# Kernel optimization log

Measured on AMD Instinct MI355X. Metric: run time of the kernel, lower is better.

The kernel has to match this reference:

```python
import jax, jax.numpy as jnp
import numpy as np

NUM_HEADS = 16
D_MODEL = 1024
D_K = D_MODEL // NUM_HEADS


def setup_inputs() -> dict:
    key = jax.random.key(0)
    ks = jax.random.split(key, 11)
    B, S, D = 1, 4096, D_MODEL
    scale = 1.0 / np.sqrt(D)
    return {
        "Q": jax.random.normal(ks[0], (B, S, D), jnp.float32),
        "K": jax.random.normal(ks[1], (B, S, D), jnp.float32),
        "V": jax.random.normal(ks[2], (B, S, D), jnp.float32),
        "W_Q": jax.random.normal(ks[3], (D, D), jnp.float32) * scale,
        "b_Q": jax.random.normal(ks[4], (D,), jnp.float32) * 0.02,
        "W_K": jax.random.normal(ks[5], (D, D), jnp.float32) * scale,
        "b_K": jax.random.normal(ks[6], (D,), jnp.float32) * 0.02,
        "W_V": jax.random.normal(ks[7], (D, D), jnp.float32) * scale,
        "b_V": jax.random.normal(ks[8], (D,), jnp.float32) * 0.02,
        "W_O": jax.random.normal(ks[9], (D, D), jnp.float32) * scale,
        "b_O": jax.random.normal(ks[10], (D,), jnp.float32) * 0.02,
    }


def _split_heads(x):
    # (B, S, D) -> (B, H, S, d_k)
    B, S, _ = x.shape
    return x.reshape(B, S, NUM_HEADS, D_K).transpose(0, 2, 1, 3)


def reference(Q, K, V, W_Q, b_Q, W_K, b_K, W_V, b_V, W_O, b_O):
    q = _split_heads(Q @ W_Q + b_Q)  # (B, H, S, d_k)
    k = _split_heads(K @ W_K + b_K)
    v = _split_heads(V @ W_V + b_V)
    inv_sqrt_dk = jnp.asarray(1.0 / np.sqrt(D_K), q.dtype)
    scores = jnp.einsum("bhqd,bhkd->bhqk", q, k) * inv_sqrt_dk  # (B, H, S, S)
    weights = jax.nn.softmax(scores, axis=-1)
    out = jnp.einsum("bhqk,bhkd->bhqd", weights, v)  # (B, H, S, d_k)
    B, _, S, _ = out.shape
    combined = out.transpose(0, 2, 1, 3).reshape(B, S, D_MODEL)
    return combined @ W_O + b_O
```

## Files before the change

### kernel.cpp

```cpp
#include <hip/hip_runtime.h>

typedef float f32x2 __attribute__((ext_vector_type(2)));
typedef float f32x4 __attribute__((ext_vector_type(4)));
typedef float f32x16 __attribute__((ext_vector_type(16)));
typedef short bf16x8 __attribute__((ext_vector_type(8)));
typedef unsigned u32x2 __attribute__((ext_vector_type(2)));
typedef unsigned short u16;

#define S_LEN 4096
#define DMODEL 1024
#define NH 16
#define DK 64

#define SCALE_Q 0.18033688f

static __device__ __forceinline__ u16 f2bf(float x) {
  union { float f; unsigned u; } v; v.f = x;
  unsigned r = v.u + 0x7fffu + ((v.u >> 16) & 1u);
  return (u16)(r >> 16);
}

static __device__ __forceinline__ float bf2f(u16 x) {
  union { unsigned u; float f; } v; v.u = ((unsigned)x) << 16;
  return v.f;
}

#if __has_builtin(__builtin_amdgcn_exp2f)
#define EXP2F __builtin_amdgcn_exp2f
#else
#define EXP2F exp2f
#endif

static __device__ __forceinline__ unsigned pkbf(float lo, float hi) {
  unsigned r;
  asm("v_cvt_pk_bf16_f32 %0, %1, %2" : "=v"(r) : "v"(lo), "v"(hi));
  return r;
}

static __device__ __forceinline__ void plswap(unsigned& a, unsigned& b, int hi) {
#if __has_builtin(__builtin_amdgcn_permlane32_swap)
  u32x2 r = __builtin_amdgcn_permlane32_swap(a, b, false, false);
  a = r.x; b = r.y;
  (void)hi;
#else
  unsigned ax = __shfl_xor(a, 32), bx = __shfl_xor(b, 32);
  unsigned na = hi ? bx : a;
  unsigned nb = hi ? b : ax;
  a = na; b = nb;
#endif
}

static __device__ __forceinline__ void gload16(const void* g, void* l) {
  void* gg = (void*)g;
  __builtin_amdgcn_global_load_lds(
      (__attribute__((address_space(1))) void*)gg,
      (__attribute__((address_space(3))) void*)l, 16, 0, 0);
}

__global__ __launch_bounds__(256) void prep(const float* __restrict__ W0,
                                            const float* __restrict__ W1,
                                            const float* __restrict__ W2,
                                            const float* __restrict__ W3,
                                            u16* __restrict__ Wt,
                                            const float* __restrict__ Q,
                                            const float* __restrict__ K,
                                            const float* __restrict__ V,
                                            u16* __restrict__ Qbf) {
  __shared__ float t[32][33];
  const int b = blockIdx.x;
  const int tid = threadIdx.x;
  if (b < 4096) {
    const int z = b >> 10;
    const int rem = b & 1023;
    const float* W = (z == 0) ? W0 : (z == 1) ? W1 : (z == 2) ? W2 : W3;
    u16* dst = Wt + (size_t)z * DMODEL * DMODEL;
    const int x = tid & 31, y = tid >> 5;
    const int n0 = (rem & 31) * 32, k0 = (rem >> 5) * 32;
#pragma unroll
    for (int i = 0; i < 4; ++i)
      t[y + 8 * i][x] = W[(size_t)(k0 + y + 8 * i) * DMODEL + n0 + x];
    __syncthreads();
#pragma unroll
    for (int i = 0; i < 4; ++i)
      dst[(size_t)(n0 + y + 8 * i) * DMODEL + k0 + x] = f2bf(t[x][y + 8 * i]);
  } else {
    const int b2 = b - 4096;
    const int z = b2 >> 10;
    const int blk = b2 & 1023;
    const float* src = (z == 0) ? Q : (z == 1) ? K : V;
    u16* dst = Qbf + (size_t)z * S_LEN * DMODEL;
    const int n8 = S_LEN * DMODEL / 8;
    for (int i = blk * 256 + tid; i < n8; i += 1024 * 256) {
      float4 a = ((const float4*)src)[2 * i];
      float4 c = ((const float4*)src)[2 * i + 1];
      union { ushort4 u[2]; int4 q; } tt;
      tt.u[0].x = f2bf(a.x); tt.u[0].y = f2bf(a.y);
      tt.u[0].z = f2bf(a.z); tt.u[0].w = f2bf(a.w);
      tt.u[1].x = f2bf(c.x); tt.u[1].y = f2bf(c.y);
      tt.u[1].z = f2bf(c.z); tt.u[1].w = f2bf(c.w);
      ((int4*)dst)[i] = tt.q;
    }
  }
}

template <int MODE>
__global__ __launch_bounds__(256) void pgemm(const u16* __restrict__ Abase,
                                             const u16* __restrict__ Btbase,
                                             const float* __restrict__ bq,
                                             const float* __restrict__ bk,
                                             const float* __restrict__ bv,
                                             void* __restrict__ outbase) {
  __shared__ __align__(16) char Al[16384];
  __shared__ __align__(16) char Bl[16384];
  const int nblk = gridDim.x, cpx = nblk >> 3;
  const int b0 = blockIdx.x;
  const int bid = (b0 & 7) * cpx + (b0 >> 3);
  const int z = (MODE == 0) ? (bid >> 8) : 0;
  const int rem = bid & 255;
  const int nb = rem & 7, mb = rem >> 3;
  const int m0 = mb * 128, n0 = nb * 128;
  const int tid = threadIdx.x, lane = tid & 63, wid = tid >> 6;
  const int l31 = lane & 31, hi = lane >> 5;
  const int wm = (wid >> 1) * 64, wn = (wid & 1) * 64;
  const char* Ab = (const char*)(Abase + (size_t)z * S_LEN * DMODEL);
  const char* Bb = (const char*)(Btbase + (size_t)z * DMODEL * DMODEL);
  const float* bias = (z == 0) ? bq : (z == 1 ? bk : bv);
  const float scale = (MODE == 0 && z == 0) ? SCALE_Q : 1.0f;

  f32x16 acc[2][2] = {};

  for (int kt = 0; kt < 16; ++kt) {
    const int kb = kt * 128;
#pragma unroll
    for (int p = 0; p < 4; ++p) {
      int lin = p * 4096 + tid * 16;
      int row = lin >> 7;
      int colg = (lin & 127) ^ ((row & 7) << 4);
      gload16(Ab + (size_t)(m0 + row) * 2048 + kb + colg,
              Al + p * 4096 + wid * 1024);
    }
#pragma unroll
    for (int p = 0; p < 4; ++p) {
      int lin = p * 4096 + tid * 16;
      int row = lin >> 7;
      int colg = (lin & 127) ^ ((row & 7) << 4);
      gload16(Bb + (size_t)(n0 + row) * 2048 + kb + colg,
              Bl + p * 4096 + wid * 1024);
    }
    __syncthreads();
#pragma unroll
    for (int ks = 0; ks < 4; ++ks) {
      bf16x8 a2[2], b2[2];
#pragma unroll
      for (int f = 0; f < 2; ++f) {
        int row = wm + f * 32 + l31;
        a2[f] = *(const bf16x8*)(Al + row * 128 +
                                 ((ks * 32 + hi * 16) ^ ((row & 7) << 4)));
      }
#pragma unroll
      for (int g = 0; g < 2; ++g) {
        int row = wn + g * 32 + l31;
        b2[g] = *(const bf16x8*)(Bl + row * 128 +
                                 ((ks * 32 + hi * 16) ^ ((row & 7) << 4)));
      }
#pragma unroll
      for (int f = 0; f < 2; ++f)
#pragma unroll
        for (int g = 0; g < 2; ++g)
          acc[f][g] =
              __builtin_amdgcn_mfma_f32_32x32x16_bf16(a2[f], b2[g], acc[f][g], 0, 0, 0);
    }
    __syncthreads();
  }

#pragma unroll
  for (int f = 0; f < 2; ++f) {
#pragma unroll
    for (int g = 0; g < 2; ++g) {
      const int col = n0 + wn + g * 32 + l31;
      const int row0 = m0 + wm + f * 32 + 4 * hi;
      const float bb = bias[col];
      if (MODE == 1) {
        float* of = (float*)outbase;
#pragma unroll
        for (int i = 0; i < 16; ++i) {
          const int row = row0 + (i & 3) + 8 * (i >> 2);
          of[(size_t)row * DMODEL + col] = acc[f][g][i] + bb;
        }
      } else if (z == 2) {
        u16* ov = (u16*)outbase + (size_t)2 * S_LEN * DMODEL;
        u16* base = ov + ((size_t)(col >> 6) * DK + (col & 63)) * S_LEN;
#pragma unroll
        for (int q2 = 0; q2 < 4; ++q2) {
          const int row = row0 + 8 * q2;
          ushort4 u;
          u.x = f2bf(acc[f][g][4 * q2 + 0] + bb);
          u.y = f2bf(acc[f][g][4 * q2 + 1] + bb);
          u.z = f2bf(acc[f][g][4 * q2 + 2] + bb);
          u.w = f2bf(acc[f][g][4 * q2 + 3] + bb);
          *(ushort4*)(base + row) = u;
        }
      } else {
        u16* oq = (u16*)outbase + (size_t)z * S_LEN * DMODEL;
#pragma unroll
        for (int i = 0; i < 16; ++i) {
          const int row = row0 + (i & 3) + 8 * (i >> 2);
          oq[((size_t)(col >> 6) * S_LEN + row) * DK + (col & 63)] =
              f2bf((acc[f][g][i] + bb) * scale);
        }
      }
    }
  }
}

__global__ __launch_bounds__(512) void attn2(const u16* __restrict__ q,
                                             const u16* __restrict__ k,
                                             const u16* __restrict__ vt,
                                             u16* __restrict__ Opart,
                                             float* __restrict__ Lpart) {
  __shared__ __align__(16) char smem[32768];
  const int bid0 = blockIdx.x;
  const int bid = (bid0 & 7) * 64 + (bid0 >> 3);
  const int h = bid >> 5;
  const int kvh = (bid >> 4) & 1;
  const int qblk = bid & 15;
  const int tid = threadIdx.x;
  const int wid = tid >> 6, lane = tid & 63;
  const int l31 = lane & 31, hi = lane >> 5;

  const char* kpb = (const char*)k + (size_t)h * S_LEN * (DK * 2);
  const char* vtb = (const char*)vt + (size_t)h * DK * (S_LEN * 2);

  const int q0w = qblk * 256 + wid * 32;
  const u16* qrow = q + ((size_t)h * S_LEN + q0w + l31) * DK;
  bf16x8 qf[4];
#pragma unroll
  for (int dt = 0; dt < 4; ++dt)
    qf[dt] = *(const bf16x8*)(qrow + dt * 16 + hi * 8);

  f32x16 o0 = {}, o1 = {};
  f32x2 lacc2 = {0.f, 0.f};

  const int woff = wid << 10;
  const int kt0 = kvh * 32;
  const int kt1 = kt0 + 32;

  const int swz = (l31 & 7) << 4;
  int dsa[4];
#pragma unroll
  for (int dt = 0; dt < 4; ++dt)
    dsa[dt] = (l31 << 7) + ((dt * 32 + hi * 16) ^ swz);

  const int lin = tid * 16;
  const int sw = lin ^ (((lin >> 7) & 7) << 4);
  const char* gk = kpb + (size_t)kt0 * 8192 + sw;
  const char* gv = vtb + (size_t)(lin >> 7) * 8192 + (size_t)kt0 * 128 + (sw & 127);

  gload16(gk, smem + woff);          gk += 8192;
  gload16(gv, smem + 8192 + woff);   gv += 128;

  auto body = [&](const int CUR, const int NXT, bool doStage) {
    if (doStage) {
      gload16(gk, smem + NXT + woff);          gk += 8192;
      gload16(gv, smem + NXT + 8192 + woff);   gv += 128;
      asm volatile("s_waitcnt vmcnt(2)" ::: "memory");
    } else {
      asm volatile("s_waitcnt vmcnt(0)" ::: "memory");
    }
    __builtin_amdgcn_s_barrier();

    const char* kb = smem + CUR;
    const char* vb = smem + CUR + 8192;

    f32x16 st0 = {}, st1 = {};
    __builtin_amdgcn_s_setprio(1);
#pragma unroll
    for (int dt = 0; dt < 4; ++dt) {
      bf16x8 k0 = *(const bf16x8*)(kb + dsa[dt]);
      bf16x8 k1 = *(const bf16x8*)(kb + 4096 + dsa[dt]);
      st0 = __builtin_amdgcn_mfma_f32_32x32x16_bf16(k0, qf[dt], st0, 0, 0, 0);
      st1 = __builtin_amdgcn_mfma_f32_32x32x16_bf16(k1, qf[dt], st1, 0, 0, 0);
    }
    __builtin_amdgcn_s_setprio(0);

    unsigned w0[8], w1[8];
    f32x2 s2 = {0.f, 0.f};
#pragma unroll
    for (int i = 0; i < 8; ++i) {
      float a0 = EXP2F(st0[2 * i]), a1 = EXP2F(st0[2 * i + 1]);
      f32x2 t = {a0, a1}; s2 += t;
      w0[i] = pkbf(a0, a1);
    }
#pragma unroll
    for (int i = 0; i < 8; ++i) {
      float a0 = EXP2F(st1[2 * i]), a1 = EXP2F(st1[2 * i + 1]);
      f32x2 t = {a0, a1}; s2 += t;
      w1[i] = pkbf(a0, a1);
    }
    lacc2 += s2;

    union UF { unsigned w[4]; bf16x8 v; };
    UF f[4];
#pragma unroll
    for (int g = 0; g < 2; ++g) {
#pragma unroll
      for (int j = 0; j < 2; ++j) {
        unsigned a = w0[4 * g + j], b = w0[4 * g + j + 2];
        plswap(a, b, hi);
        f[g].w[j] = a; f[g].w[j + 2] = b;
        unsigned c = w1[4 * g + j], d = w1[4 * g + j + 2];
        plswap(c, d, hi);
        f[2 + g].w[j] = c; f[2 + g].w[j + 2] = d;
      }
    }

    __builtin_amdgcn_s_setprio(1);
#pragma unroll
    for (int kt2 = 0; kt2 < 4; ++kt2) {
      bf16x8 v0 = *(const bf16x8*)(vb + dsa[kt2]);
      bf16x8 v1 = *(const bf16x8*)(vb + 4096 + dsa[kt2]);
      o0 = __builtin_amdgcn_mfma_f32_32x32x16_bf16(v0, f[kt2].v, o0, 0, 0, 0);
      o1 = __builtin_amdgcn_mfma_f32_32x32x16_bf16(v1, f[kt2].v, o1, 0, 0, 0);
    }
    __builtin_amdgcn_s_setprio(0);

    __builtin_amdgcn_s_barrier();
  };

  for (int kt = kt0; kt < kt1; kt += 2) {
    body(0, 16384, kt + 1 < kt1);
    body(16384, 0, kt + 2 < kt1);
  }

  const float lacc = lacc2.x + lacc2.y;
  const float lrow = lacc + __shfl_xor(lacc, 32);
  u16* Ob = Opart + ((((size_t)kvh * NH + h) * S_LEN) + q0w + l31) * DK;
#pragma unroll
  for (int g = 0; g < 4; ++g) {
    ushort4 u0, u1;
    u0.x = f2bf(o0[g * 4 + 0]); u0.y = f2bf(o0[g * 4 + 1]);
    u0.z = f2bf(o0[g * 4 + 2]); u0.w = f2bf(o0[g * 4 + 3]);
    *(ushort4*)(Ob + 8 * g + 4 * hi) = u0;
    u1.x = f2bf(o1[g * 4 + 0]); u1.y = f2bf(o1[g * 4 + 1]);
    u1.z = f2bf(o1[g * 4 + 2]); u1.w = f2bf(o1[g * 4 + 3]);
    *(ushort4*)(Ob + 32 + 8 * g + 4 * hi) = u1;
  }
  Lpart[((size_t)kvh * NH + h) * S_LEN + q0w + l31] = lrow;
}

__global__ __launch_bounds__(256) void combine(const u16* __restrict__ Op,
                                               const float* __restrict__ Lp,
                                               u16* __restrict__ comb) {
  const int id = blockIdx.x * 256 + threadIdx.x;
  const int h = id >> 16;
  const int rem = id & 65535;
  const int qv = rem >> 4;
  const int d4 = (rem & 15) << 2;
  const size_t str = (size_t)NH * S_LEN * DK;
  const size_t base = (((size_t)h * S_LEN) + qv) * DK + d4;
  float o0 = 0.f, o1 = 0.f, o2 = 0.f, o3 = 0.f, l = 0.f;
#pragma unroll
  for (int kv = 0; kv < 2; ++kv) {
    ushort4 u = *(const ushort4*)(Op + kv * str + base);
    o0 += bf2f(u.x); o1 += bf2f(u.y); o2 += bf2f(u.z); o3 += bf2f(u.w);
    l += Lp[(size_t)kv * NH * S_LEN + (size_t)h * S_LEN + qv];
  }
  const float inv = 1.f / l;
  ushort4 u;
  u.x = f2bf(o0 * inv);
  u.y = f2bf(o1 * inv);
  u.z = f2bf(o2 * inv);
  u.w = f2bf(o3 * inv);
  *(ushort4*)(comb + (size_t)qv * DMODEL + h * DK + d4) = u;
}

extern "C" void kernel_launch(void* const* d_in, const int* in_sizes, int n_in,
                              void* d_out, int out_size, void* d_ws, size_t ws_size,
                              hipStream_t stream) {
  (void)in_sizes; (void)n_in; (void)out_size; (void)ws_size;
  const float* Q   = (const float*)d_in[0];
  const float* K   = (const float*)d_in[1];
  const float* V   = (const float*)d_in[2];
  const float* W_Q = (const float*)d_in[3];
  const float* b_Q = (const float*)d_in[4];
  const float* W_K = (const float*)d_in[5];
  const float* b_K = (const float*)d_in[6];
  const float* W_V = (const float*)d_in[7];
  const float* b_V = (const float*)d_in[8];
  const float* W_O = (const float*)d_in[9];
  const float* b_O = (const float*)d_in[10];
  float* out = (float*)d_out;

  char* ws = (char*)d_ws;
  const size_t MB = 1024 * 1024;
  u16* WtQ = (u16*)ws;
  u16* Qbf = (u16*)(ws + 8 * MB);
  u16* Opart = (u16*)(ws + 8 * MB);
  u16* qp   = (u16*)(ws + 40 * MB);
  u16* kp   = qp + (size_t)S_LEN * DMODEL;
  u16* vtp  = kp + (size_t)S_LEN * DMODEL;
  u16* comb = vtp + (size_t)S_LEN * DMODEL;
  float* Lpart = (float*)(ws + 72 * MB);

  prep<<<7168, 256, 0, stream>>>(W_Q, W_K, W_V, W_O, WtQ, Q, K, V, Qbf);

  pgemm<0><<<768, 256, 0, stream>>>(Qbf, WtQ, b_Q, b_K, b_V, qp);

  attn2<<<512, 512, 0, stream>>>(qp, kp, vtp, Opart, Lpart);
  combine<<<4096, 256, 0, stream>>>(Opart, Lpart, comb);

  pgemm<1><<<256, 256, 0, stream>>>(comb, WtQ + (size_t)3 * DMODEL * DMODEL,
                                    b_O, b_O, b_O, out);
}
```

Baseline: 164.4 us.

## Double attention KV stage depth and add dedicated output-projection GEMM

The attention kernel now stages two 64-key tiles per barrier pair, using 64KB of LDS, so each pair of barriers covers twice the compute and synchronisation overhead per key is halved. Separately, the final output projection moves from the generic pgemm<1> to a new ogemm kernel with 64x128 tiles and 512 blocks, meant to fill more CUs. The larger LDS footprint may lower attention occupancy, and ogemm is not pipelined, synchronising twice per k-step.

```diff
diff --git a/kernel.cpp b/kernel.cpp
--- a/kernel.cpp
+++ b/kernel.cpp
@@ -213,12 +213,81 @@
   }
 }
 
+__global__ __launch_bounds__(256) void ogemm(const u16* __restrict__ A,
+                                             const u16* __restrict__ Bt,
+                                             const float* __restrict__ bias,
+                                             float* __restrict__ out) {
+  __shared__ __align__(16) char Al[8192];
+  __shared__ __align__(16) char Bl[16384];
+  const int b0 = blockIdx.x;
+  const int bid = (b0 & 7) * 64 + (b0 >> 3);
+  const int nb = bid & 7, mb = bid >> 3;
+  const int m0 = mb * 64, n0 = nb * 128;
+  const int tid = threadIdx.x, lane = tid & 63, wid = tid >> 6;
+  const int l31 = lane & 31, hi = lane >> 5;
+  const int wm = (wid >> 1) * 32, wn = (wid & 1) * 64;
+  const char* Ab = (const char*)A;
+  const char* Bb = (const char*)Bt;
+
+  f32x16 acc[2] = {};
+
+  for (int kt = 0; kt < 16; ++kt) {
+    const int kb = kt * 128;
+#pragma unroll
+    for (int p = 0; p < 2; ++p) {
+      int lin = p * 4096 + tid * 16;
+      int row = lin >> 7;
+      int colg = (lin & 127) ^ ((row & 7) << 4);
+      gload16(Ab + (size_t)(m0 + row) * 2048 + kb + colg,
+              Al + p * 4096 + wid * 1024);
+    }
+#pragma unroll
+    for (int p = 0; p < 4; ++p) {
+      int lin = p * 4096 + tid * 16;
+      int row = lin >> 7;
+      int colg = (lin & 127) ^ ((row & 7) << 4);
+      gload16(Bb + (size_t)(n0 + row) * 2048 + kb + colg,
+              Bl + p * 4096 + wid * 1024);
+    }
+    __syncthreads();
+#pragma unroll
+    for (int ks = 0; ks < 4; ++ks) {
+      int rowA = wm + l31;
+      bf16x8 a2 = *(const bf16x8*)(Al + rowA * 128 +
+                                   ((ks * 32 + hi * 16) ^ ((rowA & 7) << 4)));
+      bf16x8 b2[2];
+#pragma unroll
+      for (int g = 0; g < 2; ++g) {
+        int row = wn + g * 32 + l31;
+        b2[g] = *(const bf16x8*)(Bl + row * 128 +
+                                 ((ks * 32 + hi * 16) ^ ((row & 7) << 4)));
+      }
+#pragma unroll
+      for (int g = 0; g < 2; ++g)
+        acc[g] = __builtin_amdgcn_mfma_f32_32x32x16_bf16(a2, b2[g], acc[g], 0, 0, 0);
+    }
+    __syncthreads();
+  }
+
+#pragma unroll
+  for (int g = 0; g < 2; ++g) {
+    const int col = n0 + wn + g * 32 + l31;
+    const int row0 = m0 + wm + 4 * hi;
+    const float bb = bias[col];
+#pragma unroll
+    for (int i = 0; i < 16; ++i) {
+      const int row = row0 + (i & 3) + 8 * (i >> 2);
+      out[(size_t)row * DMODEL + col] = acc[g][i] + bb;
+    }
+  }
+}
+
 __global__ __launch_bounds__(512) void attn2(const u16* __restrict__ q,
                                              const u16* __restrict__ k,
                                              const u16* __restrict__ vt,
                                              u16* __restrict__ Opart,
                                              float* __restrict__ Lpart) {
-  __shared__ __align__(16) char smem[32768];
+  __shared__ __align__(16) char smem[65536];
   const int bid0 = blockIdx.x;
   const int bid = (bid0 & 7) * 64 + (bid0 >> 3);
   const int h = bid >> 5;
@@ -243,7 +312,6 @@
 
   const int woff = wid << 10;
   const int kt0 = kvh * 32;
-  const int kt1 = kt0 + 32;
 
   const int swz = (l31 & 7) << 4;
   int dsa[4];
@@ -256,22 +324,14 @@
   const char* gk = kpb + (size_t)kt0 * 8192 + sw;
   const char* gv = vtb + (size_t)(lin >> 7) * 8192 + (size_t)kt0 * 128 + (sw & 127);
 
-  gload16(gk, smem + woff);          gk += 8192;
-  gload16(gv, smem + 8192 + woff);   gv += 128;
-
-  auto body = [&](const int CUR, const int NXT, bool doStage) {
-    if (doStage) {
-      gload16(gk, smem + NXT + woff);          gk += 8192;
-      gload16(gv, smem + NXT + 8192 + woff);   gv += 128;
-      asm volatile("s_waitcnt vmcnt(2)" ::: "memory");
-    } else {
-      asm volatile("s_waitcnt vmcnt(0)" ::: "memory");
-    }
-    __builtin_amdgcn_s_barrier();
-
-    const char* kb = smem + CUR;
-    const char* vb = smem + CUR + 8192;
-
+  gload16(gk, smem + woff);           gk += 8192;
+  gload16(gv, smem + 8192 + woff);    gv += 128;
+  gload16(gk, smem + 16384 + woff);   gk += 8192;
+  gload16(gv, smem + 24576 + woff);   gv += 128;
+
+  union UF { unsigned w[4]; bf16x8 v; };
+
+  auto subtile = [&](const char* kb, const char* vb) {
     f32x16 st0 = {}, st1 = {};
     __builtin_amdgcn_s_setprio(1);
 #pragma unroll
@@ -299,7 +359,6 @@
     }
     lacc2 += s2;
 
-    union UF { unsigned w[4]; bf16x8 v; };
     UF f[4];
 #pragma unroll
     for (int g = 0; g < 2; ++g) {
@@ -323,13 +382,29 @@
       o1 = __builtin_amdgcn_mfma_f32_32x32x16_bf16(v1, f[kt2].v, o1, 0, 0, 0);
     }
     __builtin_amdgcn_s_setprio(0);
+  };
+
+  auto body = [&](const int CUR, const int NXT, bool doStage) {
+    if (doStage) {
+      gload16(gk, smem + NXT + woff);           gk += 8192;
+      gload16(gv, smem + NXT + 8192 + woff);    gv += 128;
+      gload16(gk, smem + NXT + 16384 + woff);   gk += 8192;
+      gload16(gv, smem + NXT + 24576 + woff);   gv += 128;
+      asm volatile("s_waitcnt vmcnt(4)" ::: "memory");
+    } else {
+      asm volatile("s_waitcnt vmcnt(0)" ::: "memory");
+    }
+    __builtin_amdgcn_s_barrier();
+
+    subtile(smem + CUR, smem + CUR + 8192);
+    subtile(smem + CUR + 16384, smem + CUR + 24576);
 
     __builtin_amdgcn_s_barrier();
   };
 
-  for (int kt = kt0; kt < kt1; kt += 2) {
-    body(0, 16384, kt + 1 < kt1);
-    body(16384, 0, kt + 2 < kt1);
+  for (int b2 = 0; b2 < 16; b2 += 2) {
+    body(0, 32768, b2 + 1 < 16);
+    body(32768, 0, b2 + 2 < 16);
   }
 
   const float lacc = lacc2.x + lacc2.y;
@@ -409,6 +484,6 @@
   attn2<<<512, 512, 0, stream>>>(qp, kp, vtp, Opart, Lpart);
   combine<<<4096, 256, 0, stream>>>(Opart, Lpart, comb);
 
-  pgemm<1><<<256, 256, 0, stream>>>(comb, WtQ + (size_t)3 * DMODEL * DMODEL,
-                                    b_O, b_O, b_O, out);
-}
+  ogemm<<<512, 256, 0, stream>>>(comb, WtQ + (size_t)3 * DMODEL * DMODEL,
+                                 b_O, out);
+}
```

New measurement: 161.8 us. No clear change (-1.6%).

## Double-buffer LDS in projection GEMM and add smaller-tile output GEMM

Applied to the files above, without the earlier changes.

The QKV projection GEMM now double-buffers its A/B tiles in LDS. It issues the next k-tile's global-to-LDS loads before computing the current one, with explicit vmcnt waits and barriers replacing the load-sync-compute-sync loop. The output projection moves to a dedicated kernel with 64x128 tiles and 512 blocks for better CU occupancy on the 256-tile problem, also double-buffered. LDS per block grows to 64KB and 48KB, which may limit blocks per CU, and the hand-placed waitcnt counts must match the exact load counts.

```diff
diff --git a/kernel.cpp b/kernel.cpp
--- a/kernel.cpp
+++ b/kernel.cpp
@@ -103,19 +103,17 @@
   }
 }
 
-template <int MODE>
 __global__ __launch_bounds__(256) void pgemm(const u16* __restrict__ Abase,
                                              const u16* __restrict__ Btbase,
                                              const float* __restrict__ bq,
                                              const float* __restrict__ bk,
                                              const float* __restrict__ bv,
                                              void* __restrict__ outbase) {
-  __shared__ __align__(16) char Al[16384];
-  __shared__ __align__(16) char Bl[16384];
+  __shared__ __align__(16) char smem[65536];
   const int nblk = gridDim.x, cpx = nblk >> 3;
   const int b0 = blockIdx.x;
   const int bid = (b0 & 7) * cpx + (b0 >> 3);
-  const int z = (MODE == 0) ? (bid >> 8) : 0;
+  const int z = bid >> 8;
   const int rem = bid & 255;
   const int nb = rem & 7, mb = rem >> 3;
   const int m0 = mb * 128, n0 = nb * 128;
@@ -125,29 +123,34 @@
   const char* Ab = (const char*)(Abase + (size_t)z * S_LEN * DMODEL);
   const char* Bb = (const char*)(Btbase + (size_t)z * DMODEL * DMODEL);
   const float* bias = (z == 0) ? bq : (z == 1 ? bk : bv);
-  const float scale = (MODE == 0 && z == 0) ? SCALE_Q : 1.0f;
+  const float scale = (z == 0) ? SCALE_Q : 1.0f;
 
   f32x16 acc[2][2] = {};
 
-  for (int kt = 0; kt < 16; ++kt) {
-    const int kb = kt * 128;
-#pragma unroll
-    for (int p = 0; p < 4; ++p) {
-      int lin = p * 4096 + tid * 16;
-      int row = lin >> 7;
-      int colg = (lin & 127) ^ ((row & 7) << 4);
-      gload16(Ab + (size_t)(m0 + row) * 2048 + kb + colg,
-              Al + p * 4096 + wid * 1024);
-    }
-#pragma unroll
-    for (int p = 0; p < 4; ++p) {
-      int lin = p * 4096 + tid * 16;
-      int row = lin >> 7;
-      int colg = (lin & 127) ^ ((row & 7) << 4);
-      gload16(Bb + (size_t)(n0 + row) * 2048 + kb + colg,
-              Bl + p * 4096 + wid * 1024);
-    }
-    __syncthreads();
+  float bb2[2];
+#pragma unroll
+  for (int g = 0; g < 2; ++g) bb2[g] = bias[n0 + wn + g * 32 + l31];
+  asm volatile("s_waitcnt vmcnt(0)" ::: "memory");
+
+  const int r8 = tid >> 3;
+  const int colg = ((tid * 16) & 127) ^ ((r8 & 7) << 4);
+  const char* gA = Ab + (size_t)(m0 + r8) * 2048 + colg;
+  const char* gB = Bb + (size_t)(n0 + r8) * 2048 + colg;
+  const int ldst = wid * 1024;
+
+  auto stageAB = [&](int base) {
+#pragma unroll
+    for (int p = 0; p < 4; ++p)
+      gload16(gA + p * 65536, smem + base + p * 4096 + ldst);
+#pragma unroll
+    for (int p = 0; p < 4; ++p)
+      gload16(gB + p * 65536, smem + base + 16384 + p * 4096 + ldst);
+    gA += 128; gB += 128;
+  };
+
+  auto compute = [&](int base) {
+    const char* Al = smem + base;
+    const char* Bl = smem + base + 16384;
 #pragma unroll
     for (int ks = 0; ks < 4; ++ks) {
       bf16x8 a2[2], b2[2];
@@ -170,7 +173,25 @@
           acc[f][g] =
               __builtin_amdgcn_mfma_f32_32x32x16_bf16(a2[f], b2[g], acc[f][g], 0, 0, 0);
     }
-    __syncthreads();
+  };
+
+  auto body = [&](const int CUR, const int NXT, bool doStage) {
+    __builtin_amdgcn_sched_barrier(0);
+    if (doStage) {
+      stageAB(NXT);
+      asm volatile("s_waitcnt vmcnt(8)" ::: "memory");
+    } else {
+      asm volatile("s_waitcnt vmcnt(0)" ::: "memory");
+    }
+    __builtin_amdgcn_s_barrier();
+    compute(CUR);
+    __builtin_amdgcn_s_barrier();
+  };
+
+  stageAB(0);
+  for (int kt = 0; kt < 16; kt += 2) {
+    body(0, 32768, kt + 1 < 16);
+    body(32768, 0, kt + 2 < 16);
   }
 
 #pragma unroll
@@ -179,15 +200,8 @@
     for (int g = 0; g < 2; ++g) {
       const int col = n0 + wn + g * 32 + l31;
       const int row0 = m0 + wm + f * 32 + 4 * hi;
-      const float bb = bias[col];
-      if (MODE == 1) {
-        float* of = (float*)outbase;
-#pragma unroll
-        for (int i = 0; i < 16; ++i) {
-          const int row = row0 + (i & 3) + 8 * (i >> 2);
-          of[(size_t)row * DMODEL + col] = acc[f][g][i] + bb;
-        }
-      } else if (z == 2) {
+      const float bb = bb2[g];
+      if (z == 2) {
         u16* ov = (u16*)outbase + (size_t)2 * S_LEN * DMODEL;
         u16* base = ov + ((size_t)(col >> 6) * DK + (col & 63)) * S_LEN;
 #pragma unroll
@@ -209,6 +223,95 @@
               f2bf((acc[f][g][i] + bb) * scale);
         }
       }
+    }
+  }
+}
+
+__global__ __launch_bounds__(256) void ogemm(const u16* __restrict__ A,
+                                             const u16* __restrict__ Bt,
+                                             const float* __restrict__ bias,
+                                             float* __restrict__ out) {
+  __shared__ __align__(16) char smem[49152];
+  const int b0 = blockIdx.x;
+  const int bid = (b0 & 7) * 64 + (b0 >> 3);
+  const int nb = bid & 7, mb = bid >> 3;
+  const int m0 = mb * 64, n0 = nb * 128;
+  const int tid = threadIdx.x, lane = tid & 63, wid = tid >> 6;
+  const int l31 = lane & 31, hi = lane >> 5;
+  const int wm = (wid >> 1) * 32, wn = (wid & 1) * 64;
+
+  f32x16 acc[2] = {};
+
+  float bb2[2];
+#pragma unroll
+  for (int g = 0; g < 2; ++g) bb2[g] = bias[n0 + wn + g * 32 + l31];
+  asm volatile("s_waitcnt vmcnt(0)" ::: "memory");
+
+  const int r8 = tid >> 3;
+  const int colg = ((tid * 16) & 127) ^ ((r8 & 7) << 4);
+  const char* gA = (const char*)A + (size_t)(m0 + r8) * 2048 + colg;
+  const char* gB = (const char*)Bt + (size_t)(n0 + r8) * 2048 + colg;
+  const int ldst = wid * 1024;
+
+  auto stageAB = [&](int base) {
+#pragma unroll
+    for (int p = 0; p < 2; ++p)
+      gload16(gA + p * 65536, smem + base + p * 4096 + ldst);
+#pragma unroll
+    for (int p = 0; p < 4; ++p)
+      gload16(gB + p * 65536, smem + base + 8192 + p * 4096 + ldst);
+    gA += 128; gB += 128;
+  };
+
+  auto compute = [&](int base) {
+    const char* Al = smem + base;
+    const char* Bl = smem + base + 8192;
+#pragma unroll
+    for (int ks = 0; ks < 4; ++ks) {
+      int rowA = wm + l31;
+      bf16x8 a2 = *(const bf16x8*)(Al + rowA * 128 +
+                                   ((ks * 32 + hi * 16) ^ ((rowA & 7) << 4)));
+      bf16x8 b2[2];
+#pragma unroll
+      for (int g = 0; g < 2; ++g) {
+        int row = wn + g * 32 + l31;
+        b2[g] = *(const bf16x8*)(Bl + row * 128 +
+                                 ((ks * 32 + hi * 16) ^ ((row & 7) << 4)));
+      }
+#pragma unroll
+      for (int g = 0; g < 2; ++g)
+        acc[g] = __builtin_amdgcn_mfma_f32_32x32x16_bf16(a2, b2[g], acc[g], 0, 0, 0);
+    }
+  };
+
+  auto body = [&](const int CUR, const int NXT, bool doStage) {
+    __builtin_amdgcn_sched_barrier(0);
+    if (doStage) {
+      stageAB(NXT);
+      asm volatile("s_waitcnt vmcnt(6)" ::: "memory");
+    } else {
+      asm volatile("s_waitcnt vmcnt(0)" ::: "memory");
+    }
+    __builtin_amdgcn_s_barrier();
+    compute(CUR);
+    __builtin_amdgcn_s_barrier();
+  };
+
+  stageAB(0);
+  for (int kt = 0; kt < 16; kt += 2) {
+    body(0, 24576, kt + 1 < 16);
+    body(24576, 0, kt + 2 < 16);
+  }
+
+#pragma unroll
+  for (int g = 0; g < 2; ++g) {
+    const int col = n0 + wn + g * 32 + l31;
+    const int row0 = m0 + wm + 4 * hi;
+    const float bb = bb2[g];
+#pragma unroll
+    for (int i = 0; i < 16; ++i) {
+      const int row = row0 + (i & 3) + 8 * (i >> 2);
+      out[(size_t)row * DMODEL + col] = acc[g][i] + bb;
     }
   }
 }
@@ -404,11 +507,11 @@
 
   prep<<<7168, 256, 0, stream>>>(W_Q, W_K, W_V, W_O, WtQ, Q, K, V, Qbf);
 
-  pgemm<0><<<768, 256, 0, stream>>>(Qbf, WtQ, b_Q, b_K, b_V, qp);
+  pgemm<<<768, 256, 0, stream>>>(Qbf, WtQ, b_Q, b_K, b_V, qp);
 
   attn2<<<512, 512, 0, stream>>>(qp, kp, vtp, Opart, Lpart);
   combine<<<4096, 256, 0, stream>>>(Opart, Lpart, comb);
 
-  pgemm<1><<<256, 256, 0, stream>>>(comb, WtQ + (size_t)3 * DMODEL * DMODEL,
-                                    b_O, b_O, b_O, out);
-}
+  ogemm<<<512, 256, 0, stream>>>(comb, WtQ + (size_t)3 * DMODEL * DMODEL,
+                                 b_O, out);
+}
```

Measured after the change: 154.8 us (median of 2 runs). -5.8%, faster.
